# Performance work log

Measured on AMD Instinct MI355X. Metric: run time of the kernel, lower is better.

The kernel has to match this reference:

```python
import jax, jax.numpy as jnp
import numpy as np

NUM_HEADS = 12
HEAD_DIM = 64
SCALE = HEAD_DIM ** -0.5


def setup_inputs() -> dict:
    key = jax.random.key(0)
    ks = jax.random.split(key, 5)
    B, N, C = 8, 1024, 768
    x = jax.random.normal(ks[0], (B, N, C), dtype=jnp.float32)
    qkv_w = jax.random.normal(ks[1], (3 * C, C), dtype=jnp.float32) * (C ** -0.5)
    qkv_b = jax.random.normal(ks[2], (3 * C,), dtype=jnp.float32) * 0.02
    proj_w = jax.random.normal(ks[3], (C, C), dtype=jnp.float32) * (C ** -0.5)
    proj_b = jax.random.normal(ks[4], (C,), dtype=jnp.float32) * 0.02
    return {"x": x, "qkv_w": qkv_w, "qkv_b": qkv_b, "proj_w": proj_w, "proj_b": proj_b}


def reference(x, qkv_w, qkv_b, proj_w, proj_b):
    B, N, C = x.shape
    H, D = NUM_HEADS, HEAD_DIM
    # qkv projection: (B,N,3C) -> (3,B,H,N,D)
    qkv = (x @ qkv_w.T + qkv_b).reshape(B, N, 3, H, D).transpose(2, 0, 3, 1, 4)
    q, k, v = qkv[0], qkv[1], qkv[2]
    q = q * SCALE
    # full N x N attention scores, softmax over keys
    attn = jax.nn.softmax(jnp.einsum("bhnd,bhmd->bhnm", q, k), axis=-1)
    # Libragrad: detach the softmax map before multiplying with V
    attn = jax.lax.stop_gradient(attn)
    out = jnp.einsum("bhnm,bhmd->bhnd", attn, v)  # (B,H,N,D)
    out = out.transpose(0, 2, 1, 3).reshape(B, N, C)
    return out @ proj_w.T + proj_b
```

## Files before the change

### kernel.cpp

```cpp
#include <hip/hip_runtime.h>

#define NH 12
#define HD 64
#define BB 8
#define SEQ 1024
#define CD 768

typedef __bf16 bf16x8 __attribute__((ext_vector_type(8)));
typedef float f32x4 __attribute__((ext_vector_type(4)));

__device__ __forceinline__ unsigned short f2bf(float f) {
    unsigned int u = __float_as_uint(f);
    u = (u + 0x7fffu + ((u >> 16) & 1u)) >> 16;
    return (unsigned short)u;
}

__device__ __forceinline__ void gld_lds16(const unsigned short* g, unsigned short* l) {
    __builtin_amdgcn_global_load_lds(
        (const __attribute__((address_space(1))) unsigned int*)g,
        (__attribute__((address_space(3))) unsigned int*)l, 16, 0, 0);
}

#define N4_X 1572864
#define N4_W1 442368
#define N4_W2 147456
__global__ void cast_all(const float* __restrict__ x, const float* __restrict__ w1,
                         const float* __restrict__ w2,
                         unsigned short* __restrict__ ox, unsigned short* __restrict__ ow1,
                         unsigned short* __restrict__ ow2) {
    int i = blockIdx.x * blockDim.x + threadIdx.x;
    const float4* src;
    ushort4* dst;
    if (i < N4_X) {
        src = (const float4*)x + i; dst = (ushort4*)ox + i;
    } else if (i < N4_X + N4_W1) {
        src = (const float4*)w1 + (i - N4_X); dst = (ushort4*)ow1 + (i - N4_X);
    } else if (i < N4_X + N4_W1 + N4_W2) {
        src = (const float4*)w2 + (i - N4_X - N4_W1); dst = (ushort4*)ow2 + (i - N4_X - N4_W1);
    } else return;
    float4 f = *src;
    ushort4 o;
    o.x = f2bf(f.x); o.y = f2bf(f.y); o.z = f2bf(f.z); o.w = f2bf(f.w);
    *dst = o;
}

template<int MODE>
__global__ __launch_bounds__(256)
void gemm_bt(const unsigned short* __restrict__ A, const unsigned short* __restrict__ W,
             const float* __restrict__ bias,
             unsigned short* __restrict__ qb, unsigned short* __restrict__ kb,
             unsigned short* __restrict__ vb, float* __restrict__ fout,
             int M, int N, int K) {
    __shared__ __attribute__((aligned(16))) unsigned short As[128 * 64];
    __shared__ __attribute__((aligned(16))) unsigned short Bs[128 * 64];

    const int t    = threadIdx.x;
    const int bm0  = blockIdx.x * 128;
    const int bn0  = blockIdx.y * 128;
    const int wave = t >> 6;
    const int lane = t & 63;
    const int wm   = (wave >> 1) * 64;
    const int wn   = (wave & 1) * 64;
    const int col  = lane & 15;
    const int quad = lane >> 4;

    const int srow = t >> 3;
    const int scol = (t & 7) * 8;

    f32x4 acc[4][4];
#pragma unroll
    for (int i = 0; i < 4; i++)
#pragma unroll
        for (int j = 0; j < 4; j++) acc[i][j] = (f32x4){0.f, 0.f, 0.f, 0.f};

    for (int k0 = 0; k0 < K; k0 += 64) {
        __syncthreads();
#pragma unroll
        for (int p = 0; p < 4; p++) {
            gld_lds16(A + (size_t)(bm0 + p * 32 + srow) * K + k0 + scol,
                      As + (p * 32 + srow) * 64 + scol);
            gld_lds16(W + (size_t)(bn0 + p * 32 + srow) * K + k0 + scol,
                      Bs + (p * 32 + srow) * 64 + scol);
        }
        __syncthreads();

        bf16x8 af[4][2], bf[4][2];
#pragma unroll
        for (int mi = 0; mi < 4; mi++)
#pragma unroll
            for (int h = 0; h < 2; h++)
                af[mi][h] = *(const bf16x8*)(As + (wm + mi * 16 + col) * 64 + h * 32 + quad * 8);
#pragma unroll
        for (int ni = 0; ni < 4; ni++)
#pragma unroll
            for (int h = 0; h < 2; h++)
                bf[ni][h] = *(const bf16x8*)(Bs + (wn + ni * 16 + col) * 64 + h * 32 + quad * 8);
#pragma unroll
        for (int mi = 0; mi < 4; mi++)
#pragma unroll
            for (int ni = 0; ni < 4; ni++) {
                acc[mi][ni] = __builtin_amdgcn_mfma_f32_16x16x32_bf16(
                    af[mi][0], bf[ni][0], acc[mi][ni], 0, 0, 0);
                acc[mi][ni] = __builtin_amdgcn_mfma_f32_16x16x32_bf16(
                    af[mi][1], bf[ni][1], acc[mi][ni], 0, 0, 0);
            }
    }

    if (MODE == 1) {
#pragma unroll
        for (int mi = 0; mi < 4; mi++)
#pragma unroll
            for (int ni = 0; ni < 4; ni++) {
                const int n = bn0 + wn + ni * 16 + col;
                const float bv = bias[n];
#pragma unroll
                for (int r = 0; r < 4; r++) {
                    const int m = bm0 + wm + mi * 16 + quad * 4 + r;
                    fout[(size_t)m * N + n] = acc[mi][ni][r] + bv;
                }
            }
        return;
    }

    const int sel = bn0 / 768;
    const int nb  = bn0 - sel * 768;
    const int b   = bm0 >> 10;
    const int nqb = bm0 & 1023;
    unsigned short* const dstbuf = (sel == 0) ? qb : (sel == 1) ? kb : vb;
    const float scale = (sel == 0) ? 0.18033688f : 1.0f;

#pragma unroll
    for (int ni = 0; ni < 4; ni++) {
        const int hn = nb + wn + ni * 16;
        const int h  = hn >> 6;
        const int d0 = hn & 63;
        const float bv = bias[bn0 + wn + ni * 16 + col];
        unsigned short* const rowbase =
            dstbuf + ((size_t)(b * NH + h) * SEQ) * HD + d0 + col;
#pragma unroll
        for (int mi = 0; mi < 4; mi++)
#pragma unroll
            for (int r = 0; r < 4; r++) {
                const int nq = nqb + wm + mi * 16 + quad * 4 + r;
                rowbase[(size_t)nq * HD] = f2bf((acc[mi][ni][r] + bv) * scale);
            }
    }
}

__global__ __launch_bounds__(256)
void vtrans(const unsigned short* __restrict__ v, unsigned short* __restrict__ vt) {
    __shared__ __attribute__((aligned(16))) unsigned short T[64 * 72];
    const int bh = blockIdx.x;
    const int kt = blockIdx.y;
    const int t  = threadIdx.x;
    const int r  = t >> 2;
    const int c  = (t & 3) * 16;

    const unsigned short* src = v + ((size_t)bh * SEQ + kt * 64 + r) * HD + c;
    *(uint4*)(T + r * 72 + c)     = *(const uint4*)src;
    *(uint4*)(T + r * 72 + c + 8) = *(const uint4*)(src + 8);
    __syncthreads();

    union { unsigned short us[16]; uint4 u4[2]; } o;
#pragma unroll
    for (int j = 0; j < 16; j++) o.us[j] = T[(c + j) * 72 + r];
    unsigned short* dst = vt + ((size_t)bh * HD + r) * SEQ + kt * 64 + c;
    *(uint4*)dst       = o.u4[0];
    *(uint4*)(dst + 8) = o.u4[1];
}

__global__ __launch_bounds__(256, 3)
void attn_mfma(const unsigned short* __restrict__ qb,
               const unsigned short* __restrict__ kb,
               const unsigned short* __restrict__ vb,
               unsigned short* __restrict__ ob) {
    __shared__ __attribute__((aligned(16))) unsigned short Ks[64 * 72];
    __shared__ __attribute__((aligned(16))) unsigned short VT[64 * 72];
    __shared__ __attribute__((aligned(16))) unsigned short Ps[128 * 76];

    const int t  = threadIdx.x;
    const int bh = blockIdx.x;
    const int qt = blockIdx.y;
    const size_t base = (size_t)bh * SEQ * HD;

    const int sr = t >> 2;
    const int sc = (t & 3) * 16;

    const int wave = t >> 6;
    const int lane = t & 63;
    const int col  = lane & 15;
    const int quad = lane >> 4;

    bf16x8 aq[2][2];
#pragma unroll
    for (int u = 0; u < 2; u++) {
        const int q = qt * 128 + (2 * wave + u) * 16 + col;
        aq[u][0] = *(const bf16x8*)(qb + base + (size_t)q * HD + quad * 8);
        aq[u][1] = *(const bf16x8*)(qb + base + (size_t)q * HD + 32 + quad * 8);
    }

    float l_r[2] = {0.f, 0.f};
    f32x4 accO[2][4];
#pragma unroll
    for (int u = 0; u < 2; u++)
#pragma unroll
        for (int di = 0; di < 4; di++) accO[u][di] = (f32x4){0.f, 0.f, 0.f, 0.f};

    const unsigned short* kp = kb + base + (size_t)sr * HD + sc;
    const unsigned short* vp = vb + base + (size_t)sr * SEQ + sc;
    uint4 kr0 = *(const uint4*)kp,  kr1 = *(const uint4*)(kp + 8);
    uint4 vr0 = *(const uint4*)vp,  vr1 = *(const uint4*)(vp + 8);

    for (int kc = 0; kc < 16; kc++) {
        __syncthreads();
        *(uint4*)(Ks + sr * 72 + sc)     = kr0;
        *(uint4*)(Ks + sr * 72 + sc + 8) = kr1;
        *(uint4*)(VT + sr * 72 + sc)     = vr0;
        *(uint4*)(VT + sr * 72 + sc + 8) = vr1;
        __syncthreads();

        if (kc < 15) {
            const unsigned short* kn = kp + (size_t)(kc + 1) * 64 * HD;
            const unsigned short* vn = vp + (size_t)(kc + 1) * 64;
            kr0 = *(const uint4*)kn; kr1 = *(const uint4*)(kn + 8);
            vr0 = *(const uint4*)vn; vr1 = *(const uint4*)(vn + 8);
        }

        f32x4 accT[2][4];
#pragma unroll
        for (int ni = 0; ni < 4; ni++) {
            bf16x8 bk0 = *(const bf16x8*)(Ks + (ni * 16 + col) * 72 + quad * 8);
            bf16x8 bk1 = *(const bf16x8*)(Ks + (ni * 16 + col) * 72 + 32 + quad * 8);
#pragma unroll
            for (int u = 0; u < 2; u++) {
                f32x4 z = (f32x4){0.f, 0.f, 0.f, 0.f};
                z = __builtin_amdgcn_mfma_f32_16x16x32_bf16(bk0, aq[u][0], z, 0, 0, 0);
                z = __builtin_amdgcn_mfma_f32_16x16x32_bf16(bk1, aq[u][1], z, 0, 0, 0);
                accT[u][ni] = z;
            }
        }

#pragma unroll
        for (int u = 0; u < 2; u++) {
            const int prow = (2 * wave + u) * 16;
#pragma unroll
            for (int ni = 0; ni < 4; ni++) {
                float p0 = __builtin_exp2f(accT[u][ni][0]);
                float p1 = __builtin_exp2f(accT[u][ni][1]);
                float p2 = __builtin_exp2f(accT[u][ni][2]);
                float p3 = __builtin_exp2f(accT[u][ni][3]);
                l_r[u] += (p0 + p1) + (p2 + p3);
                union { __bf16 b[4]; uint2 u2; } pk;
                pk.b[0] = (__bf16)p0; pk.b[1] = (__bf16)p1;
                pk.b[2] = (__bf16)p2; pk.b[3] = (__bf16)p3;
                *(uint2*)(Ps + (prow + col) * 76 + ni * 16 + quad * 4) = pk.u2;
            }
        }

        bf16x8 ap[2][2];
#pragma unroll
        for (int u = 0; u < 2; u++) {
            const int prow = (2 * wave + u) * 16;
            ap[u][0] = *(const bf16x8*)(Ps + (prow + col) * 76 + quad * 8);
            ap[u][1] = *(const bf16x8*)(Ps + (prow + col) * 76 + 32 + quad * 8);
        }
#pragma unroll
        for (int di = 0; di < 4; di++) {
            bf16x8 bv0 = *(const bf16x8*)(VT + (di * 16 + col) * 72 + quad * 8);
            bf16x8 bv1 = *(const bf16x8*)(VT + (di * 16 + col) * 72 + 32 + quad * 8);
#pragma unroll
            for (int u = 0; u < 2; u++) {
                accO[u][di] = __builtin_amdgcn_mfma_f32_16x16x32_bf16(ap[u][0], bv0, accO[u][di], 0, 0, 0);
                accO[u][di] = __builtin_amdgcn_mfma_f32_16x16x32_bf16(ap[u][1], bv1, accO[u][di], 0, 0, 0);
            }
        }
    }

    const int b = bh / NH, h = bh - b * NH;
#pragma unroll
    for (int u = 0; u < 2; u++) {
        float s = l_r[u];
        s += __shfl_xor(s, 16);
        s += __shfl_xor(s, 32);
#pragma unroll
        for (int r = 0; r < 4; r++) {
            const float inv = 1.f / __shfl(s, quad * 4 + r);
            const int q = qt * 128 + (2 * wave + u) * 16 + quad * 4 + r;
            const size_t rowbase = ((size_t)b * SEQ + q) * CD + h * 64;
#pragma unroll
            for (int di = 0; di < 4; di++)
                ob[rowbase + di * 16 + col] = f2bf(accO[u][di][r] * inv);
        }
    }
}

extern "C" void kernel_launch(void* const* d_in, const int* in_sizes, int n_in,
                              void* d_out, int out_size, void* d_ws, size_t ws_size,
                              hipStream_t stream) {
    const float* x      = (const float*)d_in[0];
    const float* qkv_w  = (const float*)d_in[1];
    const float* qkv_b  = (const float*)d_in[2];
    const float* proj_w = (const float*)d_in[3];
    const float* proj_b = (const float*)d_in[4];
    float* out = (float*)d_out;

    char* ws = (char*)d_ws;
    unsigned short* x_bf     = (unsigned short*)ws;
    unsigned short* qkvw_bf  = (unsigned short*)(ws + 12582912);
    unsigned short* projw_bf = (unsigned short*)(ws + 12582912 + 3538944);
    unsigned short* q_bf     = (unsigned short*)(ws + 12582912 + 3538944 + 1179648);
    unsigned short* k_bf     = q_bf + 6291456;
    unsigned short* v_bf     = k_bf + 6291456;
    unsigned short* vt_bf    = x_bf;
    unsigned short* attn_bf  = v_bf;

    cast_all<<<8448, 256, 0, stream>>>(x, qkv_w, proj_w, x_bf, qkvw_bf, projw_bf);

    gemm_bt<0><<<dim3(64, 18), 256, 0, stream>>>(x_bf, qkvw_bf, qkv_b,
                                                 q_bf, k_bf, v_bf, nullptr,
                                                 8192, 2304, 768);

    vtrans<<<dim3(96, 16), 256, 0, stream>>>(v_bf, vt_bf);

    attn_mfma<<<dim3(96, 8), 256, 0, stream>>>(q_bf, k_bf, vt_bf, attn_bf);

    gemm_bt<1><<<dim3(64, 6), 256, 0, stream>>>(attn_bf, projw_bf, proj_b,
                                                nullptr, nullptr, nullptr, out,
                                                8192, 768, 768);
}
```

Measured before the change: 214.9 us.

## Halve GEMM K-tile and attention query tile, add MFMA priority hints

The GEMM now stages 32-wide K slices instead of 64, halving shared memory per block and doubling the number of loop iterations and barriers. The attention kernel processes 64 query rows per block instead of 128, with one 16-row strip per wave, doubling the grid to 1536 blocks and raising the occupancy hint to 4. It also wraps the MFMA sections in s_setprio so waves with matrix work are scheduled ahead of others. The aim is more blocks and waves per CU to hide latency, at the cost of reloading each K/V tile for twice as many query blocks and paying more synchronisation per unit of GEMM work.

Measured after the change: 210.0 us. 1.02x faster.

```diff
diff --git a/kernel.cpp b/kernel.cpp
--- a/kernel.cpp
+++ b/kernel.cpp
@@ -51,8 +51,8 @@
              unsigned short* __restrict__ qb, unsigned short* __restrict__ kb,
              unsigned short* __restrict__ vb, float* __restrict__ fout,
              int M, int N, int K) {
-    __shared__ __attribute__((aligned(16))) unsigned short As[128 * 64];
-    __shared__ __attribute__((aligned(16))) unsigned short Bs[128 * 64];
+    __shared__ __attribute__((aligned(16))) unsigned short As[128 * 32];
+    __shared__ __attribute__((aligned(16))) unsigned short Bs[128 * 32];
 
     const int t    = threadIdx.x;
     const int bm0  = blockIdx.x * 128;
@@ -64,8 +64,8 @@
     const int col  = lane & 15;
     const int quad = lane >> 4;
 
-    const int srow = t >> 3;
-    const int scol = (t & 7) * 8;
+    const int srow = t >> 2;
+    const int scol = (t & 3) * 8;
 
     f32x4 acc[4][4];
 #pragma unroll
@@ -73,37 +73,27 @@
 #pragma unroll
         for (int j = 0; j < 4; j++) acc[i][j] = (f32x4){0.f, 0.f, 0.f, 0.f};
 
-    for (int k0 = 0; k0 < K; k0 += 64) {
+    for (int k0 = 0; k0 < K; k0 += 32) {
         __syncthreads();
-#pragma unroll
-        for (int p = 0; p < 4; p++) {
-            gld_lds16(A + (size_t)(bm0 + p * 32 + srow) * K + k0 + scol,
-                      As + (p * 32 + srow) * 64 + scol);
-            gld_lds16(W + (size_t)(bn0 + p * 32 + srow) * K + k0 + scol,
-                      Bs + (p * 32 + srow) * 64 + scol);
-        }
+        gld_lds16(A + (size_t)(bm0 + srow) * K + k0 + scol,      As + srow * 32 + scol);
+        gld_lds16(A + (size_t)(bm0 + 64 + srow) * K + k0 + scol, As + (64 + srow) * 32 + scol);
+        gld_lds16(W + (size_t)(bn0 + srow) * K + k0 + scol,      Bs + srow * 32 + scol);
+        gld_lds16(W + (size_t)(bn0 + 64 + srow) * K + k0 + scol, Bs + (64 + srow) * 32 + scol);
         __syncthreads();
 
-        bf16x8 af[4][2], bf[4][2];
+        bf16x8 af[4], bf[4];
 #pragma unroll
         for (int mi = 0; mi < 4; mi++)
-#pragma unroll
-            for (int h = 0; h < 2; h++)
-                af[mi][h] = *(const bf16x8*)(As + (wm + mi * 16 + col) * 64 + h * 32 + quad * 8);
+            af[mi] = *(const bf16x8*)(As + (wm + mi * 16 + col) * 32 + quad * 8);
 #pragma unroll
         for (int ni = 0; ni < 4; ni++)
-#pragma unroll
-            for (int h = 0; h < 2; h++)
-                bf[ni][h] = *(const bf16x8*)(Bs + (wn + ni * 16 + col) * 64 + h * 32 + quad * 8);
+            bf[ni] = *(const bf16x8*)(Bs + (wn + ni * 16 + col) * 32 + quad * 8);
 #pragma unroll
         for (int mi = 0; mi < 4; mi++)
 #pragma unroll
-            for (int ni = 0; ni < 4; ni++) {
+            for (int ni = 0; ni < 4; ni++)
                 acc[mi][ni] = __builtin_amdgcn_mfma_f32_16x16x32_bf16(
-                    af[mi][0], bf[ni][0], acc[mi][ni], 0, 0, 0);
-                acc[mi][ni] = __builtin_amdgcn_mfma_f32_16x16x32_bf16(
-                    af[mi][1], bf[ni][1], acc[mi][ni], 0, 0, 0);
-            }
+                    af[mi], bf[ni], acc[mi][ni], 0, 0, 0);
     }
 
     if (MODE == 1) {
@@ -169,14 +159,14 @@
     *(uint4*)(dst + 8) = o.u4[1];
 }
 
-__global__ __launch_bounds__(256, 3)
+__global__ __launch_bounds__(256, 4)
 void attn_mfma(const unsigned short* __restrict__ qb,
                const unsigned short* __restrict__ kb,
                const unsigned short* __restrict__ vb,
                unsigned short* __restrict__ ob) {
     __shared__ __attribute__((aligned(16))) unsigned short Ks[64 * 72];
     __shared__ __attribute__((aligned(16))) unsigned short VT[64 * 72];
-    __shared__ __attribute__((aligned(16))) unsigned short Ps[128 * 76];
+    __shared__ __attribute__((aligned(16))) unsigned short Ps[64 * 76];
 
     const int t  = threadIdx.x;
     const int bh = blockIdx.x;
@@ -191,25 +181,24 @@
     const int col  = lane & 15;
     const int quad = lane >> 4;
 
-    bf16x8 aq[2][2];
-#pragma unroll
-    for (int u = 0; u < 2; u++) {
-        const int q = qt * 128 + (2 * wave + u) * 16 + col;
-        aq[u][0] = *(const bf16x8*)(qb + base + (size_t)q * HD + quad * 8);
-        aq[u][1] = *(const bf16x8*)(qb + base + (size_t)q * HD + 32 + quad * 8);
-    }
-
-    float l_r[2] = {0.f, 0.f};
-    f32x4 accO[2][4];
-#pragma unroll
-    for (int u = 0; u < 2; u++)
-#pragma unroll
-        for (int di = 0; di < 4; di++) accO[u][di] = (f32x4){0.f, 0.f, 0.f, 0.f};
+    bf16x8 aq0, aq1;
+    {
+        const int q = qt * 64 + wave * 16 + col;
+        aq0 = *(const bf16x8*)(qb + base + (size_t)q * HD + quad * 8);
+        aq1 = *(const bf16x8*)(qb + base + (size_t)q * HD + 32 + quad * 8);
+    }
+
+    float l_r = 0.f;
+    f32x4 accO[4];
+#pragma unroll
+    for (int di = 0; di < 4; di++) accO[di] = (f32x4){0.f, 0.f, 0.f, 0.f};
 
     const unsigned short* kp = kb + base + (size_t)sr * HD + sc;
     const unsigned short* vp = vb + base + (size_t)sr * SEQ + sc;
     uint4 kr0 = *(const uint4*)kp,  kr1 = *(const uint4*)(kp + 8);
     uint4 vr0 = *(const uint4*)vp,  vr1 = *(const uint4*)(vp + 8);
+
+    const int prow = wave * 16;
 
     for (int kc = 0; kc < 16; kc++) {
         __syncthreads();
@@ -226,71 +215,57 @@
             vr0 = *(const uint4*)vn; vr1 = *(const uint4*)(vn + 8);
         }
 
-        f32x4 accT[2][4];
+        f32x4 accT[4];
+        __builtin_amdgcn_s_setprio(1);
 #pragma unroll
         for (int ni = 0; ni < 4; ni++) {
             bf16x8 bk0 = *(const bf16x8*)(Ks + (ni * 16 + col) * 72 + quad * 8);
             bf16x8 bk1 = *(const bf16x8*)(Ks + (ni * 16 + col) * 72 + 32 + quad * 8);
-#pragma unroll
-            for (int u = 0; u < 2; u++) {
-                f32x4 z = (f32x4){0.f, 0.f, 0.f, 0.f};
-                z = __builtin_amdgcn_mfma_f32_16x16x32_bf16(bk0, aq[u][0], z, 0, 0, 0);
-                z = __builtin_amdgcn_mfma_f32_16x16x32_bf16(bk1, aq[u][1], z, 0, 0, 0);
-                accT[u][ni] = z;
-            }
+            f32x4 z = (f32x4){0.f, 0.f, 0.f, 0.f};
+            z = __builtin_amdgcn_mfma_f32_16x16x32_bf16(bk0, aq0, z, 0, 0, 0);
+            z = __builtin_amdgcn_mfma_f32_16x16x32_bf16(bk1, aq1, z, 0, 0, 0);
+            accT[ni] = z;
         }
-
-#pragma unroll
-        for (int u = 0; u < 2; u++) {
-            const int prow = (2 * wave + u) * 16;
-#pragma unroll
-            for (int ni = 0; ni < 4; ni++) {
-                float p0 = __builtin_exp2f(accT[u][ni][0]);
-                float p1 = __builtin_exp2f(accT[u][ni][1]);
-                float p2 = __builtin_exp2f(accT[u][ni][2]);
-                float p3 = __builtin_exp2f(accT[u][ni][3]);
-                l_r[u] += (p0 + p1) + (p2 + p3);
-                union { __bf16 b[4]; uint2 u2; } pk;
-                pk.b[0] = (__bf16)p0; pk.b[1] = (__bf16)p1;
-                pk.b[2] = (__bf16)p2; pk.b[3] = (__bf16)p3;
-                *(uint2*)(Ps + (prow + col) * 76 + ni * 16 + quad * 4) = pk.u2;
-            }
+        __builtin_amdgcn_s_setprio(0);
+
+#pragma unroll
+        for (int ni = 0; ni < 4; ni++) {
+            float p0 = __builtin_exp2f(accT[ni][0]);
+            float p1 = __builtin_exp2f(accT[ni][1]);
+            float p2 = __builtin_exp2f(accT[ni][2]);
+            float p3 = __builtin_exp2f(accT[ni][3]);
+            l_r += (p0 + p1) + (p2 + p3);
+            union { __bf16 b[4]; uint2 u2; } pk;
+            pk.b[0] = (__bf16)p0; pk.b[1] = (__bf16)p1;
+            pk.b[2] = (__bf16)p2; pk.b[3] = (__bf16)p3;
+            *(uint2*)(Ps + (prow + col) * 76 + ni * 16 + quad * 4) = pk.u2;
         }
 
-        bf16x8 ap[2][2];
-#pragma unroll
-        for (int u = 0; u < 2; u++) {
-            const int prow = (2 * wave + u) * 16;
-            ap[u][0] = *(const bf16x8*)(Ps + (prow + col) * 76 + quad * 8);
-            ap[u][1] = *(const bf16x8*)(Ps + (prow + col) * 76 + 32 + quad * 8);
-        }
+        bf16x8 ap0 = *(const bf16x8*)(Ps + (prow + col) * 76 + quad * 8);
+        bf16x8 ap1 = *(const bf16x8*)(Ps + (prow + col) * 76 + 32 + quad * 8);
+        __builtin_amdgcn_s_setprio(1);
 #pragma unroll
         for (int di = 0; di < 4; di++) {
             bf16x8 bv0 = *(const bf16x8*)(VT + (di * 16 + col) * 72 + quad * 8);
             bf16x8 bv1 = *(const bf16x8*)(VT + (di * 16 + col) * 72 + 32 + quad * 8);
-#pragma unroll
-            for (int u = 0; u < 2; u++) {
-                accO[u][di] = __builtin_amdgcn_mfma_f32_16x16x32_bf16(ap[u][0], bv0, accO[u][di], 0, 0, 0);
-                accO[u][di] = __builtin_amdgcn_mfma_f32_16x16x32_bf16(ap[u][1], bv1, accO[u][di], 0, 0, 0);
-            }
+            accO[di] = __builtin_amdgcn_mfma_f32_16x16x32_bf16(ap0, bv0, accO[di], 0, 0, 0);
+            accO[di] = __builtin_amdgcn_mfma_f32_16x16x32_bf16(ap1, bv1, accO[di], 0, 0, 0);
         }
+        __builtin_amdgcn_s_setprio(0);
     }
 
     const int b = bh / NH, h = bh - b * NH;
-#pragma unroll
-    for (int u = 0; u < 2; u++) {
-        float s = l_r[u];
-        s += __shfl_xor(s, 16);
-        s += __shfl_xor(s, 32);
-#pragma unroll
-        for (int r = 0; r < 4; r++) {
-            const float inv = 1.f / __shfl(s, quad * 4 + r);
-            const int q = qt * 128 + (2 * wave + u) * 16 + quad * 4 + r;
-            const size_t rowbase = ((size_t)b * SEQ + q) * CD + h * 64;
-#pragma unroll
-            for (int di = 0; di < 4; di++)
-                ob[rowbase + di * 16 + col] = f2bf(accO[u][di][r] * inv);
-        }
+    float s = l_r;
+    s += __shfl_xor(s, 16);
+    s += __shfl_xor(s, 32);
+#pragma unroll
+    for (int r = 0; r < 4; r++) {
+        const float inv = 1.f / __shfl(s, quad * 4 + r);
+        const int q = qt * 64 + wave * 16 + quad * 4 + r;
+        const size_t rowbase = ((size_t)b * SEQ + q) * CD + h * 64;
+#pragma unroll
+        for (int di = 0; di < 4; di++)
+            ob[rowbase + di * 16 + col] = f2bf(accO[di][r] * inv);
     }
 }
 
@@ -322,7 +297,7 @@
 
     vtrans<<<dim3(96, 16), 256, 0, stream>>>(v_bf, vt_bf);
 
-    attn_mfma<<<dim3(96, 8), 256, 0, stream>>>(q_bf, k_bf, vt_bf, attn_bf);
+    attn_mfma<<<dim3(96, 16), 256, 0, stream>>>(q_bf, k_bf, vt_bf, attn_bf);
 
     gemm_bt<1><<<dim3(64, 6), 256, 0, stream>>>(attn_bf, projw_bf, proj_b,
                                                 nullptr, nullptr, nullptr, out,
```
